# Kernel tuning notes

Measured on AMD Instinct MI355X. Metric: run time of the kernel, lower is better.

The kernel has to match this reference:

```python
import jax, jax.numpy as jnp
import numpy as np

N_LAYERS = 200
KSIZE = 7
L_IN = 1388
FC_IN = 188   # 1388 - 200*6
FC_OUT = 91


def setup_inputs() -> dict:
    key = jax.random.key(0)
    k_x, k_w, k_b, k_fw, k_fb = jax.random.split(key, 5)
    B = 1024
    x = jax.random.normal(k_x, (B, L_IN), dtype=jnp.float32)
    # Conv1d(1,1,7) weights: torch default init U(-s, s) with s = 1/sqrt(in_ch*k) = 1/sqrt(7)
    s = 1.0 / np.sqrt(KSIZE)
    conv_w = jax.random.uniform(k_w, (N_LAYERS, KSIZE), dtype=jnp.float32, minval=-s, maxval=s)
    conv_b = jax.random.uniform(k_b, (N_LAYERS,), dtype=jnp.float32, minval=-s, maxval=s)
    sf = 1.0 / np.sqrt(FC_IN)
    fc_w = jax.random.uniform(k_fw, (FC_OUT, FC_IN), dtype=jnp.float32, minval=-sf, maxval=sf)
    fc_b = jax.random.uniform(k_fb, (FC_OUT,), dtype=jnp.float32, minval=-sf, maxval=sf)
    return {"x": x, "conv_w": conv_w, "conv_b": conv_b, "fc_w": fc_w, "fc_b": fc_b}


def _conv1(h, w, b):
    # h: [B, L]; cross-correlation with taps w[0..6], valid padding -> [B, L-6]
    L_out = h.shape[1] - (KSIZE - 1)
    acc = w[0] * h[:, 0:L_out]
    for k in range(1, KSIZE):
        acc = acc + w[k] * h[:, k:k + L_out]
    return acc + b


def reference(x, conv_w, conv_b, fc_w, fc_b):
    h = x  # unsqueeze(1) is implicit: single channel handled as [B, L]
    for i in range(N_LAYERS):
        h = _conv1(h, conv_w[i], conv_b[i])
        if i < N_LAYERS - 1:  # last ReLU was popped in the torch module
            h = jax.nn.relu(h)
    # Linear(188, 91) applied to the length dim, then Sigmoid; squeeze channel dim
    out = jax.nn.sigmoid(h @ fc_w.T + fc_b)  # [B, 91]
    return out
```

## Files before the change

### kernel.cpp

```cpp
#include <hip/hip_runtime.h>
#include <math.h>

#define N_LAYERS 200
#define KSIZE 7
#define L_IN 1388
#define FC_IN 188
#define FC_OUT 91
#define NT 256
#define NSTAGES 13
#define LBUF_N 1376

typedef float v2f __attribute__((ext_vector_type(2)));

constexpr int s_lo(int s)  { return 16 * s; }
constexpr int s_hi(int s)  { return (s < 12) ? 16 * s + 16 : N_LAYERS; }
constexpr int lin_(int s)  { return L_IN - 6 * s_lo(s); }
constexpr int lout_(int s) { return L_IN - 6 * s_hi(s); }
constexpr int cut_(int s)  { return lout_(s) / 2; }
constexpr int marg_(int s) { return 6 * (s_hi(s) - s_lo(s)); }
constexpr int s_R(int s) {
    const int a = cut_(s) + marg_(s);
    const int b = lin_(s) - cut_(s);
    const int m = (a > b) ? a : b;
    return (m + 63) / 64;
}
constexpr int s_Re(int s) { return (s_R(s) + 1) & ~1; }

__device__ __forceinline__ float dpp_next(float v) {
    return __int_as_float(
        __builtin_amdgcn_mov_dpp(__float_as_int(v), 0x130, 0xf, 0xf, true));
}
__device__ __forceinline__ v2f dpp_next2(v2f v) {
    v2f o; o.x = dpp_next(v.x); o.y = dpp_next(v.y); return o;
}

__device__ __forceinline__ v2f pk_fma(v2f a, v2f b, v2f c) {
    return __builtin_elementwise_fma(a, b, c);
}
__device__ __forceinline__ v2f pk_max0(v2f a) {
    return __builtin_elementwise_max(a, (v2f)(0.0f));
}

struct WG { v2f w2[28]; v2f b2[4]; };

__device__ __forceinline__ void load_wg(WG& wg, const v2f* wbuf2,
                                        const v2f* bbuf2, int g) {
#pragma unroll
    for (int t = 0; t < 28; ++t) wg.w2[t] = wbuf2[g * 28 + t];
#pragma unroll
    for (int j = 0; j < 4; ++j) wg.b2[j] = bbuf2[g * 4 + j];
}

template<int R, bool NR3>
__device__ __forceinline__ void run4(v2f (&r2)[6], const WG& wg) {
    constexpr int P = R / 2;
#pragma unroll
    for (int jj = 0; jj < 4; ++jj) {
        v2f C[6];
        {
            constexpr int NC = (P < 6) ? P : 6;
#pragma unroll
            for (int t = 0; t < NC; ++t) {
                v2f c; c.x = r2[t].y; c.y = dpp_next(r2[t].x);
                C[t] = c;
            }
#pragma unroll
            for (int t = NC; t < 6; ++t) C[t] = dpp_next2(C[t - P]);
        }
        const bool relu = !(NR3 && jj == 3);
#pragma unroll
        for (int j = 0; j < P; ++j) {
            v2f acc = wg.b2[jj];
#pragma unroll
            for (int d = 0; d < KSIZE; ++d) {
                const int m = j + d;
                const v2f src = (m < P) ? r2[m] : C[m - P];
                acc = pk_fma(wg.w2[jj * 7 + d], src, acc);
            }
            r2[j] = relu ? pk_max0(acc) : acc;
        }
    }
}

template<int R, bool FINAL>
__device__ __forceinline__ void run_stage_g(v2f (&r2)[6], WG& A,
        const v2f* wbuf2, const v2f* bbuf2, int g0, int g1) {
#pragma unroll 1
    for (int g = g0; g < g1; g += 2) {
        WG B;
        load_wg(B, wbuf2, bbuf2, (g + 1 < 50) ? g + 1 : 49);
        run4<R, false>(r2, A);
        load_wg(A, wbuf2, bbuf2, (g + 2 < 50) ? g + 2 : 49);
        run4<R, FINAL>(r2, B);
    }
}

template<int Ro, int Rn>
__device__ __forceinline__ void repack(v2f (&r2)[6], float* lb,
                                       int lane, int rwid,
                                       int cut_o, int lout_o, int cut_n)
{
    constexpr int Po = Ro / 2, Pn = Rn / 2;
    const int base  = rwid ? cut_o : 0;
    const int bound = rwid ? lout_o : cut_o;
    const int o = base + lane * Ro;
#pragma unroll
    for (int j = 0; j < Po; ++j) {
        if (o + j < bound)      lb[o + j]      = r2[j].x;
        if (o + j + Po < bound) lb[o + j + Po] = r2[j].y;
    }
    __syncthreads();
    const int nb = (rwid ? cut_n : 0) + lane * Rn;
#pragma unroll
    for (int j = 0; j < Pn; ++j) {
        v2f v; v.x = lb[nb + j]; v.y = lb[nb + j + Pn];
        r2[j] = v;
    }
    __syncthreads();
}

template<int S>
struct Chain {
    __device__ static __forceinline__ void run(v2f (&r2)[6], WG& A,
        const v2f* wbuf2, const v2f* bbuf2, float* lbufr, int lane, int rwid)
    {
        run_stage_g<s_Re(S), false>(r2, A, wbuf2, bbuf2, 4 * S, 4 * S + 4);
        repack<s_Re(S), s_Re(S + 1)>(r2, lbufr, lane, rwid,
                                     cut_(S), lout_(S), cut_(S + 1));
        Chain<S + 1>::run(r2, A, wbuf2, bbuf2, lbufr, lane, rwid);
    }
};

template<>
struct Chain<NSTAGES - 1> {
    __device__ static __forceinline__ void run(v2f (&r2)[6], WG& A,
        const v2f* wbuf2, const v2f* bbuf2, float* lbufr, int lane, int rwid)
    {
        constexpr int R = s_Re(NSTAGES - 1);
        constexpr int P = R / 2;
        run_stage_g<R, true>(r2, A, wbuf2, bbuf2, 48, 50);
        const int base  = rwid ? 94 : 0;
        const int bound = rwid ? 188 : 94;
        const int o = base + lane * R;
#pragma unroll
        for (int j = 0; j < P; ++j) {
            if (o + j < bound)     lbufr[o + j]     = r2[j].x;
            if (o + j + P < bound) lbufr[o + j + P] = r2[j].y;
        }
        __syncthreads();
    }
};

__global__ __launch_bounds__(NT, 2) void conv_chain_kernel(
    const float* __restrict__ x,
    const float* __restrict__ conv_w,
    const float* __restrict__ conv_b,
    const float* __restrict__ fc_w,
    const float* __restrict__ fc_b,
    float* __restrict__ out)
{
    __shared__ __align__(16) float lbuf[2][LBUF_N];
    __shared__ __align__(16) v2f wbuf2[N_LAYERS * KSIZE];
    __shared__ __align__(16) v2f bbuf2[N_LAYERS];

    const int tid   = threadIdx.x;
    const int lane  = tid & 63;
    const int wid   = tid >> 6;
    const int rsel  = wid >> 1;
    const int rwid  = wid & 1;
    const int row   = blockIdx.x * 2 + rsel;

    float* lbufr = lbuf[rsel];

    for (int i = tid; i < N_LAYERS * KSIZE; i += NT) {
        const float v = conv_w[i];
        v2f p; p.x = v; p.y = v; wbuf2[i] = p;
    }
    for (int i = tid; i < N_LAYERS; i += NT) {
        const float v = conv_b[i];
        v2f p; p.x = v; p.y = v; bbuf2[i] = p;
    }
    for (int i = tid; i < 2 * LBUF_N; i += NT) lbuf[0][i] = 0.0f;

    v2f r2[6];
    const float* xr = x + (size_t)row * L_IN;
    constexpr int R0 = s_Re(0), P0 = R0 / 2;
    const int c0 = rwid ? cut_(0) : 0;
    const int o0 = c0 + lane * R0;
#pragma unroll
    for (int j = 0; j < P0; ++j) {
        const int pa = o0 + j, pb = o0 + j + P0;
        v2f v;
        v.x = (pa < L_IN) ? xr[pa] : 0.0f;
        v.y = (pb < L_IN) ? xr[pb] : 0.0f;
        r2[j] = v;
    }
    __syncthreads();

    WG A;
    load_wg(A, wbuf2, bbuf2, 0);

    Chain<0>::run(r2, A, wbuf2, bbuf2, lbufr, lane, rwid);

    const int pt = tid & 127;
    if (pt < FC_OUT) {
        float acc = fc_b[pt];
        const float4* wp = (const float4*)(fc_w + pt * FC_IN);
        const float4* hp = (const float4*)lbufr;
#pragma unroll 4
        for (int q = 0; q < FC_IN / 4; ++q) {
            const float4 hv = hp[q];
            const float4 wv = wp[q];
            acc = fmaf(wv.x, hv.x, acc);
            acc = fmaf(wv.y, hv.y, acc);
            acc = fmaf(wv.z, hv.z, acc);
            acc = fmaf(wv.w, hv.w, acc);
        }
        out[(size_t)row * FC_OUT + pt] = 1.0f / (1.0f + expf(-acc));
    }
}

extern "C" void kernel_launch(void* const* d_in, const int* in_sizes, int n_in,
                              void* d_out, int out_size, void* d_ws, size_t ws_size,
                              hipStream_t stream) {
    const float* x      = (const float*)d_in[0];
    const float* conv_w = (const float*)d_in[1];
    const float* conv_b = (const float*)d_in[2];
    const float* fc_w   = (const float*)d_in[3];
    const float* fc_b   = (const float*)d_in[4];
    float* outp = (float*)d_out;

    const int batch = in_sizes[0] / L_IN;
    conv_chain_kernel<<<batch / 2, NT, 0, stream>>>(x, conv_w, conv_b, fc_w, fc_b, outp);
}
```

Measured before the change: 114.0 us.

## Assign one row per wavefront and drop block-wide barriers in repack

Each batch row is now handled by a single 64-lane wavefront instead of two wavefronts splitting the row with overlapping halo margins. This removes the redundant halo computation and the __syncthreads calls between stages; repacking goes through a per-wave LDS buffer, uses sched_barrier only, and is skipped when the per-lane width does not change. The cost is up to 11 register pairs per lane, which means more VGPR pressure, and launch bounds are lowered to one block per CU. The grid is now batch/4 blocks of four rows each.

```diff
diff --git a/kernel.cpp b/kernel.cpp
--- a/kernel.cpp
+++ b/kernel.cpp
@@ -8,23 +8,11 @@
 #define FC_OUT 91
 #define NT 256
 #define NSTAGES 13
-#define LBUF_N 1376
 
 typedef float v2f __attribute__((ext_vector_type(2)));
 
-constexpr int s_lo(int s)  { return 16 * s; }
-constexpr int s_hi(int s)  { return (s < 12) ? 16 * s + 16 : N_LAYERS; }
-constexpr int lin_(int s)  { return L_IN - 6 * s_lo(s); }
-constexpr int lout_(int s) { return L_IN - 6 * s_hi(s); }
-constexpr int cut_(int s)  { return lout_(s) / 2; }
-constexpr int marg_(int s) { return 6 * (s_hi(s) - s_lo(s)); }
-constexpr int s_R(int s) {
-    const int a = cut_(s) + marg_(s);
-    const int b = lin_(s) - cut_(s);
-    const int m = (a > b) ? a : b;
-    return (m + 63) / 64;
-}
-constexpr int s_Re(int s) { return (s_R(s) + 1) & ~1; }
+constexpr int w_in(int s) { return L_IN - 96 * s; }
+constexpr int s_P(int s)  { return (w_in(s) + 127) / 128; }
 
 __device__ __forceinline__ float dpp_next(float v) {
     return __int_as_float(
@@ -51,9 +39,8 @@
     for (int j = 0; j < 4; ++j) wg.b2[j] = bbuf2[g * 4 + j];
 }
 
-template<int R, bool NR3>
-__device__ __forceinline__ void run4(v2f (&r2)[6], const WG& wg) {
-    constexpr int P = R / 2;
+template<int P, bool NR3>
+__device__ __forceinline__ void run4(v2f (&r2)[11], const WG& wg) {
 #pragma unroll
     for (int jj = 0; jj < 4; ++jj) {
         v2f C[6];
@@ -82,76 +69,67 @@
     }
 }
 
-template<int R, bool FINAL>
-__device__ __forceinline__ void run_stage_g(v2f (&r2)[6], WG& A,
+template<int P, bool FINAL>
+__device__ __forceinline__ void run_stage_g(v2f (&r2)[11], WG& A,
         const v2f* wbuf2, const v2f* bbuf2, int g0, int g1) {
 #pragma unroll 1
     for (int g = g0; g < g1; g += 2) {
         WG B;
         load_wg(B, wbuf2, bbuf2, (g + 1 < 50) ? g + 1 : 49);
-        run4<R, false>(r2, A);
+        run4<P, false>(r2, A);
         load_wg(A, wbuf2, bbuf2, (g + 2 < 50) ? g + 2 : 49);
-        run4<R, FINAL>(r2, B);
-    }
-}
-
-template<int Ro, int Rn>
-__device__ __forceinline__ void repack(v2f (&r2)[6], float* lb,
-                                       int lane, int rwid,
-                                       int cut_o, int lout_o, int cut_n)
-{
-    constexpr int Po = Ro / 2, Pn = Rn / 2;
-    const int base  = rwid ? cut_o : 0;
-    const int bound = rwid ? lout_o : cut_o;
-    const int o = base + lane * Ro;
+        run4<P, FINAL>(r2, B);
+    }
+}
+
+template<int Po, int Pn>
+__device__ __forceinline__ void repack(v2f (&r2)[11], float* lb, int lane) {
+    const int o = lane * 2 * Po;
 #pragma unroll
     for (int j = 0; j < Po; ++j) {
-        if (o + j < bound)      lb[o + j]      = r2[j].x;
-        if (o + j + Po < bound) lb[o + j + Po] = r2[j].y;
-    }
-    __syncthreads();
-    const int nb = (rwid ? cut_n : 0) + lane * Rn;
+        lb[o + j]      = r2[j].x;
+        lb[o + j + Po] = r2[j].y;
+    }
+    __builtin_amdgcn_sched_barrier(0);
+    const int n = lane * 2 * Pn;
 #pragma unroll
     for (int j = 0; j < Pn; ++j) {
-        v2f v; v.x = lb[nb + j]; v.y = lb[nb + j + Pn];
+        v2f v; v.x = lb[n + j]; v.y = lb[n + j + Pn];
         r2[j] = v;
     }
-    __syncthreads();
 }
 
 template<int S>
 struct Chain {
-    __device__ static __forceinline__ void run(v2f (&r2)[6], WG& A,
-        const v2f* wbuf2, const v2f* bbuf2, float* lbufr, int lane, int rwid)
+    __device__ static __forceinline__ void run(v2f (&r2)[11], WG& A,
+        const v2f* wbuf2, const v2f* bbuf2, float* lbw, int lane)
     {
-        run_stage_g<s_Re(S), false>(r2, A, wbuf2, bbuf2, 4 * S, 4 * S + 4);
-        repack<s_Re(S), s_Re(S + 1)>(r2, lbufr, lane, rwid,
-                                     cut_(S), lout_(S), cut_(S + 1));
-        Chain<S + 1>::run(r2, A, wbuf2, bbuf2, lbufr, lane, rwid);
+        run_stage_g<s_P(S), false>(r2, A, wbuf2, bbuf2, 4 * S, 4 * S + 4);
+        if constexpr (s_P(S + 1) != s_P(S)) {
+            repack<s_P(S), s_P(S + 1)>(r2, lbw, lane);
+        }
+        Chain<S + 1>::run(r2, A, wbuf2, bbuf2, lbw, lane);
     }
 };
 
 template<>
 struct Chain<NSTAGES - 1> {
-    __device__ static __forceinline__ void run(v2f (&r2)[6], WG& A,
-        const v2f* wbuf2, const v2f* bbuf2, float* lbufr, int lane, int rwid)
+    __device__ static __forceinline__ void run(v2f (&r2)[11], WG& A,
+        const v2f* wbuf2, const v2f* bbuf2, float* lbw, int lane)
     {
-        constexpr int R = s_Re(NSTAGES - 1);
-        constexpr int P = R / 2;
-        run_stage_g<R, true>(r2, A, wbuf2, bbuf2, 48, 50);
-        const int base  = rwid ? 94 : 0;
-        const int bound = rwid ? 188 : 94;
-        const int o = base + lane * R;
+        constexpr int P = s_P(NSTAGES - 1);
+        run_stage_g<P, true>(r2, A, wbuf2, bbuf2, 48, 50);
+        const int o = lane * 2 * P;
 #pragma unroll
         for (int j = 0; j < P; ++j) {
-            if (o + j < bound)     lbufr[o + j]     = r2[j].x;
-            if (o + j + P < bound) lbufr[o + j + P] = r2[j].y;
-        }
-        __syncthreads();
+            lbw[o + j]     = r2[j].x;
+            lbw[o + j + P] = r2[j].y;
+        }
+        __builtin_amdgcn_sched_barrier(0);
     }
 };
 
-__global__ __launch_bounds__(NT, 2) void conv_chain_kernel(
+__global__ __launch_bounds__(NT, 1) void conv_chain_kernel(
     const float* __restrict__ x,
     const float* __restrict__ conv_w,
     const float* __restrict__ conv_b,
@@ -159,18 +137,16 @@
     const float* __restrict__ fc_b,
     float* __restrict__ out)
 {
-    __shared__ __align__(16) float lbuf[2][LBUF_N];
+    __shared__ __align__(16) float lbuf[4][1408];
     __shared__ __align__(16) v2f wbuf2[N_LAYERS * KSIZE];
     __shared__ __align__(16) v2f bbuf2[N_LAYERS];
 
-    const int tid   = threadIdx.x;
-    const int lane  = tid & 63;
-    const int wid   = tid >> 6;
-    const int rsel  = wid >> 1;
-    const int rwid  = wid & 1;
-    const int row   = blockIdx.x * 2 + rsel;
-
-    float* lbufr = lbuf[rsel];
+    const int tid  = threadIdx.x;
+    const int lane = tid & 63;
+    const int wid  = tid >> 6;
+    const int row  = blockIdx.x * 4 + wid;
+
+    float* lbw = lbuf[wid];
 
     for (int i = tid; i < N_LAYERS * KSIZE; i += NT) {
         const float v = conv_w[i];
@@ -180,13 +156,11 @@
         const float v = conv_b[i];
         v2f p; p.x = v; p.y = v; bbuf2[i] = p;
     }
-    for (int i = tid; i < 2 * LBUF_N; i += NT) lbuf[0][i] = 0.0f;
-
-    v2f r2[6];
+
+    v2f r2[11];
     const float* xr = x + (size_t)row * L_IN;
-    constexpr int R0 = s_Re(0), P0 = R0 / 2;
-    const int c0 = rwid ? cut_(0) : 0;
-    const int o0 = c0 + lane * R0;
+    constexpr int P0 = s_P(0);
+    const int o0 = lane * 2 * P0;
 #pragma unroll
     for (int j = 0; j < P0; ++j) {
         const int pa = o0 + j, pb = o0 + j + P0;
@@ -200,13 +174,12 @@
     WG A;
     load_wg(A, wbuf2, bbuf2, 0);
 
-    Chain<0>::run(r2, A, wbuf2, bbuf2, lbufr, lane, rwid);
-
-    const int pt = tid & 127;
-    if (pt < FC_OUT) {
-        float acc = fc_b[pt];
-        const float4* wp = (const float4*)(fc_w + pt * FC_IN);
-        const float4* hp = (const float4*)lbufr;
+    Chain<0>::run(r2, A, wbuf2, bbuf2, lbw, lane);
+
+    for (int oidx = lane; oidx < FC_OUT; oidx += 64) {
+        float acc = fc_b[oidx];
+        const float4* wp = (const float4*)(fc_w + oidx * FC_IN);
+        const float4* hp = (const float4*)lbw;
 #pragma unroll 4
         for (int q = 0; q < FC_IN / 4; ++q) {
             const float4 hv = hp[q];
@@ -216,7 +189,7 @@
             acc = fmaf(wv.z, hv.z, acc);
             acc = fmaf(wv.w, hv.w, acc);
         }
-        out[(size_t)row * FC_OUT + pt] = 1.0f / (1.0f + expf(-acc));
+        out[(size_t)row * FC_OUT + oidx] = 1.0f / (1.0f + expf(-acc));
     }
 }
 
@@ -231,5 +204,5 @@
     float* outp = (float*)d_out;
 
     const int batch = in_sizes[0] / L_IN;
-    conv_chain_kernel<<<batch / 2, NT, 0, stream>>>(x, conv_w, conv_b, fc_w, fc_b, outp);
-}
+    conv_chain_kernel<<<batch / 4, NT, 0, stream>>>(x, conv_w, conv_b, fc_w, fc_b, outp);
+}
```

After: 113.3 us. About the same (-0.6%).
